# Kernel optimization log

Measured on AMD Instinct MI355X. Metric: run time of the kernel, lower is better.

Reference implementation:

```python
import jax, jax.numpy as jnp
import numpy as np

B, T, C, H = 4, 2048, 2048, 16
DH = C // H  # 128

def setup_inputs() -> dict:
    key = jax.random.key(0)
    ks = jax.random.split(key, 5)
    s_in = 1.0 / np.sqrt(C)
    return {
        "x": jax.random.normal(ks[0], (B, T, C), dtype=jnp.float32),
        "qkv_w": jax.random.uniform(ks[1], (3 * C, C), jnp.float32, -s_in, s_in),
        "qkv_b": jax.random.uniform(ks[2], (3 * C,), jnp.float32, -s_in, s_in),
        "proj_w": jax.random.uniform(ks[3], (C, C), jnp.float32, -s_in, s_in),
        "proj_b": jax.random.uniform(ks[4], (C,), jnp.float32, -s_in, s_in),
    }

def reference(x, qkv_w, qkv_b, proj_w, proj_b):
    b, t, _ = x.shape
    qkv = x @ qkv_w.T + qkv_b                     # [B,T,3C]
    q, k, v = jnp.split(qkv, 3, axis=-1)
    # [B,T,C] -> [B,H,T,Dh]
    q = q.reshape(b, t, H, DH).transpose(0, 2, 1, 3)
    k = k.reshape(b, t, H, DH).transpose(0, 2, 1, 3)
    v = v.reshape(b, t, H, DH).transpose(0, 2, 1, 3)
    scores = jnp.einsum('bhqd,bhkd->bhqk', q, k) / jnp.sqrt(jnp.float32(DH))
    causal = jnp.tril(jnp.ones((t, t), dtype=bool))  # [T,T]
    scores = jnp.where(causal[None, None], scores, jnp.finfo(scores.dtype).min)
    att = jax.nn.softmax(scores, axis=-1)
    out = jnp.einsum('bhqk,bhkd->bhqd', att, v)   # [B,H,T,Dh]
    out = out.transpose(0, 2, 1, 3).reshape(b, t, C)
    return out @ proj_w.T + proj_b
```

## Files before the change

kernel.cpp:

```cpp
#include <hip/hip_runtime.h>
#include <stdint.h>


typedef __attribute__((ext_vector_type(8))) short bf8_t;
typedef __attribute__((ext_vector_type(4))) float f4_t;

__device__ __forceinline__ short f2bf(float f) {
  union { float f; uint32_t u; } x; x.f = f;
  uint32_t r = x.u + 0x7fffu + ((x.u >> 16) & 1u);
  return (short)(r >> 16);
}

#define GLD16(gp, lp) __builtin_amdgcn_global_load_lds( \
    (const __attribute__((address_space(1))) void*)(gp), \
    (__attribute__((address_space(3))) void*)(lp), 16, 0, 0)

__device__ __forceinline__ bf8_t dsr(uint32_t a) {
  bf8_t d;
  asm volatile("ds_read_b128 %0, %1" : "=v"(d) : "v"(a));
  return d;
}

#define QSCALE (0.08838834764831845f * 1.4426950408889634f)

__global__ __launch_bounds__(256) void cast3_f32_bf16(
    const float* __restrict__ a, const float* __restrict__ b,
    const float* __restrict__ c, short* __restrict__ oa,
    short* __restrict__ ob, short* __restrict__ oc,
    int na4, int nb4, int nc4) {
  int i = blockIdx.x * blockDim.x + threadIdx.x;
  const float* src; short* dst; int idx;
  if (i < na4) { src = a; dst = oa; idx = i; }
  else if (i < na4 + nb4) { src = b; dst = ob; idx = i - na4; }
  else if (i < na4 + nb4 + nc4) { src = c; dst = oc; idx = i - na4 - nb4; }
  else return;
  float4 v = ((const float4*)src)[idx];
  short4 o;
  o.x = f2bf(v.x); o.y = f2bf(v.y); o.z = f2bf(v.z); o.w = f2bf(v.w);
  ((short4*)dst)[idx] = o;
}


#define BARR() do { __builtin_amdgcn_s_barrier(); \
                    __builtin_amdgcn_sched_barrier(0); } while (0)
#define WAITDS() do { asm volatile("s_waitcnt lgkmcnt(0)" ::: "memory"); \
                      __builtin_amdgcn_sched_barrier(0); } while (0)
#define PR1 __builtin_amdgcn_s_setprio(1)
#define PR0 __builtin_amdgcn_s_setprio(0)

#define STAGE(g, loff) do { \
    GLD16((g) + voff0, ldsc + (loff) + dst0); \
    GLD16((g) + voff1, ldsc + (loff) + 8192 + dst0); } while (0)

#define QUAD(CI, CJ, AF, BF)                                                \
  if (!swapAB) {                                                            \
    _Pragma("unroll") for (int kk = 0; kk < 2; ++kk)                        \
    _Pragma("unroll") for (int i = 0; i < 4; ++i)                           \
    _Pragma("unroll") for (int j = 0; j < 2; ++j)                           \
      acc[(CI) + i][(CJ) + j] = __builtin_amdgcn_mfma_f32_16x16x32_bf16(    \
          AF[i][kk], BF[j][kk], acc[(CI) + i][(CJ) + j], 0, 0, 0);          \
  } else {                                                                  \
    _Pragma("unroll") for (int kk = 0; kk < 2; ++kk)                        \
    _Pragma("unroll") for (int i = 0; i < 4; ++i)                           \
    _Pragma("unroll") for (int j = 0; j < 2; ++j)                           \
      acc[(CI) + i][(CJ) + j] = __builtin_amdgcn_mfma_f32_16x16x32_bf16(    \
          BF[j][kk], AF[i][kk], acc[(CI) + i][(CJ) + j], 0, 0, 0);          \
  }

template <int MODE>
__global__ __launch_bounds__(512, 2) void gemm_bt(
    const short* __restrict__ A, const short* __restrict__ Bw,
    const float* __restrict__ bias, float* __restrict__ Cout,
    short* __restrict__ Qo, short* __restrict__ Ko, short* __restrict__ Vo,
    int M, int N, int K) {
  __shared__ __attribute__((aligned(16))) char lds[131072];
  const int tid = threadIdx.x;
  const int lane = tid & 63, wave = tid >> 6;
  const int quad = lane >> 4, l16 = lane & 15;
  const int wm = wave >> 2, wn = wave & 3;

  const int nwg = gridDim.x;
  const int cpx = nwg >> 3;
  const int bid = blockIdx.x;
  const int swz = (bid & 7) * cpx + (bid >> 3);
  const int nbx = N >> 8;
  const int bm = swz / nbx, bn = swz - bm * nbx;
  const int m0 = bm << 8, n0 = bn << 8;

  const int which = (MODE == 0) ? (n0 >> 11) : -1;
  const bool swapAB = (MODE == 0) && (which == 2);


  f4_t acc[8][4];
  if (!swapAB) {
#pragma unroll
    for (int j = 0; j < 4; ++j) {
      const float b0 = bias[n0 + (j >> 1) * 128 + wn * 32 + (j & 1) * 16 + l16];
      const f4_t bv = {b0, b0, b0, b0};
#pragma unroll
      for (int i = 0; i < 8; ++i) acc[i][j] = bv;
    }
  } else {
#pragma unroll
    for (int j = 0; j < 4; ++j)
#pragma unroll
      for (int r = 0; r < 4; ++r) {
        const float b0 =
            bias[n0 + (j >> 1) * 128 + wn * 32 + (j & 1) * 16 + quad * 4 + r];
#pragma unroll
        for (int i = 0; i < 8; ++i) acc[i][j][r] = b0;
      }
  }

  const char* baseA = (const char*)(A + (size_t)m0 * K);
  const char* baseB = (const char*)(Bw + (size_t)n0 * K);
  const size_t hK = (size_t)K << 8;
  const int r0 = tid >> 3;
  const int lg = (tid & 7) ^ (r0 & 7);
  const uint32_t voff0 = (uint32_t)(r0 * K + lg * 8) * 2u;
  const uint32_t voff1 = voff0 + ((uint32_t)K << 7);
  char* ldsc = (char*)lds;
  const int dst0 = tid * 16;

  const int x7 = l16 & 7;
  const int gx0 = (quad ^ x7) << 4;
  const int gx1 = ((quad | 4) ^ x7) << 4;
  const uint32_t lbase =
      (uint32_t)(uintptr_t)(__attribute__((address_space(3))) char*)lds;
  const uint32_t aAg0 = lbase + wm * 8192 + l16 * 128 + gx0;
  const uint32_t aAg1 = lbase + wm * 8192 + l16 * 128 + gx1;
  const uint32_t bBg0 = lbase + 32768 + wn * 4096 + l16 * 128 + gx0;
  const uint32_t bBg1 = lbase + 32768 + wn * 4096 + l16 * 128 + gx1;

  asm volatile("s_waitcnt vmcnt(0)" ::: "memory");
  __builtin_amdgcn_sched_barrier(0);

  STAGE(baseA, 0);
  STAGE(baseB + hK, 49152);
  STAGE(baseA + hK, 16384);
  STAGE(baseB, 32768);
  STAGE(baseA + 128, 65536 + 0);
  STAGE(baseB + hK + 128, 65536 + 49152);
  STAGE(baseA + hK + 128, 65536 + 16384);
  asm volatile("s_waitcnt vmcnt(6)" ::: "memory");
  __builtin_amdgcn_sched_barrier(0);
  __builtin_amdgcn_s_barrier();

  const int NT = K >> 6;
  bf8_t af[4][2], b0f[2][2], b1f[2][2];
  for (int t = 0; t < NT; ++t) {
    const uint32_t s = (uint32_t)(t & 1) << 16;
    const int o = (int)(s ^ 65536u);
    const size_t c1 = (size_t)(t + 1 < NT ? t + 1 : NT - 1) << 7;
    const size_t c2 = (size_t)(t + 2 < NT ? t + 2 : NT - 1) << 7;
    const uint32_t sA0 = aAg0 + s, sA1 = aAg1 + s;
    const uint32_t sB0 = bBg0 + s, sB1 = bBg1 + s;

#pragma unroll
    for (int i = 0; i < 4; ++i) {
      af[i][0] = dsr(sA0 + i * 2048);
      af[i][1] = dsr(sA1 + i * 2048);
    }
#pragma unroll
    for (int j = 0; j < 2; ++j) {
      b0f[j][0] = dsr(sB0 + j * 2048);
      b0f[j][1] = dsr(sB1 + j * 2048);
    }
    STAGE(baseB + c1, o + 32768);
    __builtin_amdgcn_s_barrier();
    WAITDS();
    PR1; QUAD(0, 0, af, b0f); PR0;
    BARR();

#pragma unroll
    for (int j = 0; j < 2; ++j) {
      b1f[j][0] = dsr(sB0 + 16384 + j * 2048);
      b1f[j][1] = dsr(sB1 + 16384 + j * 2048);
    }
    STAGE(baseA + c2, (int)s + 0);
    __builtin_amdgcn_s_barrier();
    WAITDS();
    PR1; QUAD(0, 2, af, b1f); PR0;
    BARR();

#pragma unroll
    for (int i = 0; i < 4; ++i) {
      af[i][0] = dsr(sA0 + 16384 + i * 2048);
      af[i][1] = dsr(sA1 + 16384 + i * 2048);
    }
    STAGE(baseB + hK + c2, (int)s + 49152);
    __builtin_amdgcn_s_barrier();
    WAITDS();
    PR1; QUAD(4, 2, af, b1f); PR0;
    BARR();

    STAGE(baseA + hK + c2, (int)s + 16384);
    __builtin_amdgcn_s_barrier();
    PR1; QUAD(4, 0, af, b0f); PR0;
    asm volatile("s_waitcnt vmcnt(6)" ::: "memory");
    __builtin_amdgcn_sched_barrier(0);
    __builtin_amdgcn_s_barrier();
  }

  if (MODE == 1) {
#pragma unroll
    for (int i = 0; i < 8; ++i) {
      const int mg = m0 + (i >> 2) * 128 + wm * 64 + (i & 3) * 16 + quad * 4;
#pragma unroll
      for (int r = 0; r < 4; ++r) {
        const size_t mrow = (size_t)(mg + r) * N;
#pragma unroll
        for (int j = 0; j < 4; ++j) {
          const int ng = n0 + (j >> 1) * 128 + wn * 32 + (j & 1) * 16 + l16;
          Cout[mrow + ng] = acc[i][j][r];
        }
      }
    }
  } else if (!swapAB) {
    short* dst = (which == 0) ? Qo : Ko;
    const float sc = (which == 0) ? QSCALE : 1.0f;
#pragma unroll
    for (int i = 0; i < 8; ++i) {
      const int mg = m0 + (i >> 2) * 128 + wm * 64 + (i & 3) * 16 + quad * 4;
#pragma unroll
      for (int r = 0; r < 4; ++r) {
        const int m = mg + r;
        const int b = m >> 11, tt = m & 2047;
#pragma unroll
        for (int j = 0; j < 4; ++j) {
          const int ng = n0 + (j >> 1) * 128 + wn * 32 + (j & 1) * 16 + l16;
          const int h = (ng & 2047) >> 7, d = ng & 127;
          dst[((size_t)((b * 16 + h) * 2048 + tt)) * 128 + d] =
              f2bf(acc[i][j][r] * sc);
        }
      }
    }
  } else {
#pragma unroll
    for (int i = 0; i < 8; ++i) {
      const int mg = m0 + (i >> 2) * 128 + wm * 64 + (i & 3) * 16 + l16;
      const int b = mg >> 11, tt = mg & 2047;
#pragma unroll
      for (int j = 0; j < 4; ++j) {
        const int nb = n0 + (j >> 1) * 128 + wn * 32 + (j & 1) * 16 + quad * 4;
#pragma unroll
        for (int r = 0; r < 4; ++r) {
          const int ng = nb + r;
          const int h = (ng & 2047) >> 7, d = ng & 127;
          Vo[((size_t)((b * 16 + h) * 128 + d)) * 2048 + tt] =
              f2bf(acc[i][j][r]);
        }
      }
    }
  }
}

__global__ __launch_bounds__(256) void attn_fwd(
    const short* __restrict__ Qg, const short* __restrict__ Kg,
    const short* __restrict__ Vtg, short* __restrict__ Og) {
  __shared__ __attribute__((aligned(16))) short lK[64 * 128];
  __shared__ __attribute__((aligned(16))) short lV[128 * 64];
  __shared__ __attribute__((aligned(16))) short lP[4 * 2048];
  const int tid = threadIdx.x;
  const int lane = tid & 63, wave = tid >> 6;
  const int quad = lane >> 4, l16 = lane & 15;
  const int p = blockIdx.x & 7, bh = blockIdx.x >> 3;
  const size_t baseK = (size_t)bh * (2048 * 128);
  const size_t baseV = (size_t)bh * (128 * 2048);
  const int x7 = l16 & 7;
  const int b = bh >> 4, h = bh & 15;
  short* lPw = lP + wave * 2048;
  const f4_t fz = {0.f, 0.f, 0.f, 0.f};

  uint32_t vK[4], vV[4];
#pragma unroll
  for (int r = 0; r < 4; ++r) {
    const int off = tid * 16 + r * 4096;
    const int rowK = off >> 8;
    const int lcK = ((off >> 4) & 15) ^ (rowK & 7);
    vK[r] = (uint32_t)(rowK * 128 + lcK * 8) * 2u;
    const int dV = off >> 7;
    const int lcV = ((off >> 4) & 7) ^ (dV & 7);
    vV[r] = (uint32_t)(dV * 2048 + lcV * 8) * 2u;
  }

  for (int job = 0; job < 2; ++job) {
    const int bx = job ? (15 - p) : p;
    const int q0 = bx * 128;
    const int qw = q0 + wave * 32;

    bf8_t qf[2][4];
#pragma unroll
    for (int m = 0; m < 2; ++m)
#pragma unroll
      for (int dc = 0; dc < 4; ++dc)
        qf[m][dc] = *(const bf8_t*)(Qg + baseK + (size_t)(qw + m * 16 + l16) * 128 + dc * 32 + quad * 8);

    f4_t o[2][8];
#pragma unroll
    for (int m = 0; m < 2; ++m)
#pragma unroll
      for (int n = 0; n < 8; ++n) o[m][n] = fz;
    float lsum[2][4];
#pragma unroll
    for (int m = 0; m < 2; ++m)
#pragma unroll
      for (int r = 0; r < 4; ++r) lsum[m][r] = 0.f;

    const char* kbase = (const char*)(Kg + baseK);
    const char* vbase = (const char*)(Vtg + baseV);
    const int ktmax = 2 * bx + 1;
    for (int kt = 0; kt <= ktmax; ++kt) {
      const int k0 = kt * 64;
      __syncthreads();
#pragma unroll
      for (int r = 0; r < 4; ++r) {
        const int off = tid * 16 + r * 4096;
        GLD16(kbase + vK[r], (char*)lK + off);
        GLD16(vbase + vV[r], (char*)lV + off);
      }
      kbase += 16384;
      vbase += 128;
      __syncthreads();
      if (k0 >= qw + 32) continue;

      f4_t s[2][4];
#pragma unroll
      for (int m = 0; m < 2; ++m)
#pragma unroll
        for (int g = 0; g < 4; ++g) s[m][g] = fz;
#pragma unroll
      for (int g = 0; g < 4; ++g)
#pragma unroll
        for (int dc = 0; dc < 4; ++dc) {
          bf8_t kf = *(const bf8_t*)(lK + (g * 16 + l16) * 128 + (((dc * 4 + quad) ^ x7) << 3));
          s[0][g] = __builtin_amdgcn_mfma_f32_16x16x32_bf16(qf[0][dc], kf, s[0][g], 0, 0, 0);
          s[1][g] = __builtin_amdgcn_mfma_f32_16x16x32_bf16(qf[1][dc], kf, s[1][g], 0, 0, 0);
        }
#pragma unroll
      for (int m = 0; m < 2; ++m) {
        const int qbase = qw + m * 16;
        const bool nomask = (k0 + 63 <= qbase);
#pragma unroll
        for (int g = 0; g < 4; ++g) {
          const int key = k0 + g * 16 + l16;
#pragma unroll
          for (int r = 0; r < 4; ++r) {
            float pv = exp2f(s[m][g][r]);
            if (!nomask && key > qbase + quad * 4 + r) pv = 0.f;
            lsum[m][r] += pv;
            const int row = quad * 4 + r;
            lPw[m * 1024 + row * 64 + (((g * 2 + (l16 >> 3)) ^ (row & 7)) << 3) + x7] = f2bf(pv);
          }
        }
      }
      bf8_t pa[2][2];
#pragma unroll
      for (int m = 0; m < 2; ++m)
#pragma unroll
        for (int kc = 0; kc < 2; ++kc)
          pa[m][kc] = *(const bf8_t*)(lPw + m * 1024 + l16 * 64 + (((kc * 4 + quad) ^ x7) << 3));
#pragma unroll
      for (int n = 0; n < 8; ++n)
#pragma unroll
        for (int kc = 0; kc < 2; ++kc) {
          bf8_t vf = *(const bf8_t*)(lV + (n * 16 + l16) * 64 + (((kc * 4 + quad) ^ x7) << 3));
          o[0][n] = __builtin_amdgcn_mfma_f32_16x16x32_bf16(pa[0][kc], vf, o[0][n], 0, 0, 0);
          o[1][n] = __builtin_amdgcn_mfma_f32_16x16x32_bf16(pa[1][kc], vf, o[1][n], 0, 0, 0);
        }
    }
#pragma unroll
    for (int m = 0; m < 2; ++m)
#pragma unroll
      for (int r = 0; r < 4; ++r) {
        float v = lsum[m][r];
        v += __shfl_xor(v, 1, 64);
        v += __shfl_xor(v, 2, 64);
        v += __shfl_xor(v, 4, 64);
        v += __shfl_xor(v, 8, 64);
        const float inv = 1.f / v;
        const int t = qw + m * 16 + quad * 4 + r;
        const size_t orow = ((size_t)(b * 2048 + t)) * 2048 + h * 128;
#pragma unroll
        for (int n = 0; n < 8; ++n)
          Og[orow + n * 16 + l16] = f2bf(o[m][n][r] * inv);
      }
  }
}

extern "C" void kernel_launch(void* const* d_in, const int* in_sizes, int n_in,
                              void* d_out, int out_size, void* d_ws, size_t ws_size,
                              hipStream_t stream) {
  const float* x      = (const float*)d_in[0];
  const float* qkv_w  = (const float*)d_in[1];
  const float* qkv_b  = (const float*)d_in[2];
  const float* proj_w = (const float*)d_in[3];
  const float* proj_b = (const float*)d_in[4];
  float* out = (float*)d_out;

  char* ws = (char*)d_ws;
  short* xb    = (short*)(ws);
  short* wqkv  = (short*)(ws + 33554432);
  short* wproj = (short*)(ws + 58720256);
  short* qb    = (short*)(ws + 67108864);
  short* kb    = (short*)(ws + 100663296);
  short* vb    = (short*)(ws + 134217728);
  short* attb  = (short*)(ws + 167772160);

  cast3_f32_bf16<<<32768, 256, 0, stream>>>(x, qkv_w, proj_w, xb, wqkv, wproj,
                                            4194304, 3145728, 1048576);

  gemm_bt<0><<<768, 512, 0, stream>>>(xb, wqkv, qkv_b, nullptr,
                                      qb, kb, vb, 8192, 6144, 2048);
  attn_fwd<<<512, 256, 0, stream>>>(qb, kb, vb, attb);
  gemm_bt<1><<<256, 512, 0, stream>>>(attb, wproj, proj_b, out,
                                      nullptr, nullptr, nullptr, 8192, 2048, 2048);
}
```

Baseline: 554.4 us.

## Prefetch next A fragments across iterations and remap attention block order

The GEMM main loop now uses a second A-fragment register set, so the first A fragments of the next K-tile are read from LDS during the last quadrant of the current iteration instead of at the top of the loop. This overlaps LDS reads with MFMA work. The initial staging order is also adjusted and a full wait is added after the loop. Separately, the attention kernel remaps blockIdx so that consecutive blocks belong to different batch-heads rather than to the same head. This changes L2 locality and load balance, since causal work differs between query chunks. The extra fragment registers could raise register pressure.

```diff
diff --git a/kernel.cpp b/kernel.cpp
--- a/kernel.cpp
+++ b/kernel.cpp
@@ -136,9 +136,9 @@
   __builtin_amdgcn_sched_barrier(0);
 
   STAGE(baseA, 0);
+  STAGE(baseB, 32768);
   STAGE(baseB + hK, 49152);
   STAGE(baseA + hK, 16384);
-  STAGE(baseB, 32768);
   STAGE(baseA + 128, 65536 + 0);
   STAGE(baseB + hK + 128, 65536 + 49152);
   STAGE(baseA + hK + 128, 65536 + 16384);
@@ -147,26 +147,28 @@
   __builtin_amdgcn_s_barrier();
 
   const int NT = K >> 6;
-  bf8_t af[4][2], b0f[2][2], b1f[2][2];
+  bf8_t af[4][2], af2[4][2], b0f[2][2], b1f[2][2];
+
+#pragma unroll
+  for (int i = 0; i < 4; ++i) {
+    af[i][0] = dsr(aAg0 + i * 2048);
+    af[i][1] = dsr(aAg1 + i * 2048);
+  }
+
   for (int t = 0; t < NT; ++t) {
     const uint32_t s = (uint32_t)(t & 1) << 16;
-    const int o = (int)(s ^ 65536u);
+    const uint32_t o = s ^ 65536u;
     const size_t c1 = (size_t)(t + 1 < NT ? t + 1 : NT - 1) << 7;
     const size_t c2 = (size_t)(t + 2 < NT ? t + 2 : NT - 1) << 7;
     const uint32_t sA0 = aAg0 + s, sA1 = aAg1 + s;
     const uint32_t sB0 = bBg0 + s, sB1 = bBg1 + s;
 
 #pragma unroll
-    for (int i = 0; i < 4; ++i) {
-      af[i][0] = dsr(sA0 + i * 2048);
-      af[i][1] = dsr(sA1 + i * 2048);
-    }
-#pragma unroll
     for (int j = 0; j < 2; ++j) {
       b0f[j][0] = dsr(sB0 + j * 2048);
       b0f[j][1] = dsr(sB1 + j * 2048);
     }
-    STAGE(baseB + c1, o + 32768);
+    STAGE(baseB + c1, (int)o + 32768);
     __builtin_amdgcn_s_barrier();
     WAITDS();
     PR1; QUAD(0, 0, af, b0f); PR0;
@@ -185,22 +187,30 @@
 
 #pragma unroll
     for (int i = 0; i < 4; ++i) {
-      af[i][0] = dsr(sA0 + 16384 + i * 2048);
-      af[i][1] = dsr(sA1 + 16384 + i * 2048);
+      af2[i][0] = dsr(sA0 + 16384 + i * 2048);
+      af2[i][1] = dsr(sA1 + 16384 + i * 2048);
     }
     STAGE(baseB + hK + c2, (int)s + 49152);
     __builtin_amdgcn_s_barrier();
     WAITDS();
-    PR1; QUAD(4, 2, af, b1f); PR0;
+    PR1; QUAD(4, 2, af2, b1f); PR0;
     BARR();
 
     STAGE(baseA + hK + c2, (int)s + 16384);
-    __builtin_amdgcn_s_barrier();
-    PR1; QUAD(4, 0, af, b0f); PR0;
     asm volatile("s_waitcnt vmcnt(6)" ::: "memory");
     __builtin_amdgcn_sched_barrier(0);
     __builtin_amdgcn_s_barrier();
-  }
+#pragma unroll
+    for (int i = 0; i < 4; ++i) {
+      af[i][0] = dsr(o + aAg0 + i * 2048);
+      af[i][1] = dsr(o + aAg1 + i * 2048);
+    }
+    PR1; QUAD(4, 0, af2, b0f); PR0;
+    BARR();
+  }
+
+  asm volatile("s_waitcnt vmcnt(0) lgkmcnt(0)" ::: "memory");
+  __builtin_amdgcn_sched_barrier(0);
 
   if (MODE == 1) {
 #pragma unroll
@@ -264,7 +274,9 @@
   const int tid = threadIdx.x;
   const int lane = tid & 63, wave = tid >> 6;
   const int quad = lane >> 4, l16 = lane & 15;
-  const int p = blockIdx.x & 7, bh = blockIdx.x >> 3;
+  const int bid = blockIdx.x;
+  const int bh = ((bid & 7) << 3) | ((bid >> 3) & 7);
+  const int p = bid >> 6;
   const size_t baseK = (size_t)bh * (2048 * 128);
   const size_t baseV = (size_t)bh * (128 * 2048);
   const int x7 = l16 & 7;
```

New measurement: 768.3 us. 38.6% more time.
